# Kernel tuning notes

Hardware: AMD Instinct MI355X
Metric: run time of the kernel (lower is better)

## Reference

```python
import jax, jax.numpy as jnp
import numpy as np

HIDDEN = 1024
NUM_EXPERTS = 64
N_TOKENS = 131072


def setup_inputs() -> dict:
    key = jax.random.key(0)
    k_h, k_w1, k_w2 = jax.random.split(key, 3)
    s1 = 1.0 / np.sqrt(HIDDEN)
    return {
        "h": jax.random.normal(k_h, (N_TOKENS, HIDDEN), dtype=jnp.float32),
        "W1": jax.random.uniform(k_w1, (HIDDEN, HIDDEN), minval=-s1, maxval=s1, dtype=jnp.float32),
        "b1": jnp.zeros((HIDDEN,), jnp.float32),
        "W2": jax.random.uniform(k_w2, (NUM_EXPERTS, HIDDEN), minval=-s1, maxval=s1, dtype=jnp.float32),
        "b2": jnp.zeros((NUM_EXPERTS,), jnp.float32),
        "epoch": 5,
        "top_k": 2,
        "warmup_epochs": 0,
    }


def reference(h, W1, b1, W2, b2, epoch, top_k, warmup_epochs):
    # logits = layer2(tanh(layer1(h)))  -- torch Linear stores weight [out, in]
    logits = jnp.tanh(h @ W1.T + b1) @ W2.T + b2  # [N, E]
    if epoch is None or top_k is None or epoch < warmup_epochs or top_k <= 0:
        return jax.nn.softmax(logits, axis=-1)
    k = min(top_k, NUM_EXPERTS)
    topk_vals, topk_idx = jax.lax.top_k(logits, k)  # [N, k]
    n = logits.shape[0]
    mask = jnp.zeros_like(logits).at[jnp.arange(n)[:, None], topk_idx].set(1.0)
    masked_logits = jnp.where(mask == 0, -jnp.inf, logits)
    return jax.nn.softmax(masked_logits, axis=-1)
```

## Files before the change

### kernel.cpp

```cpp
#include <hip/hip_runtime.h>


constexpr int KT         = 32;
constexpr int A_STRIDE   = 65;
constexpr int W2S_STRIDE = 68;
constexpr int W2S_OFF    = 256 * A_STRIDE;
constexpr int SMEM_FLOATS = W2S_OFF + KT * W2S_STRIDE;

constexpr int WS_B = 0;
constexpr int HS_B = 32768;

constexpr int F32_HS_STRIDE  = 68;
constexpr int F32_WS_STRIDE  = 324;
constexpr int F32_HS_OFF   = 0;
constexpr int F32_WS_OFF   = KT * F32_HS_STRIDE;

typedef __attribute__((ext_vector_type(8))) _Float16 half8;
typedef __attribute__((ext_vector_type(4))) float f32x4;

__device__ __forceinline__ float fast_tanh(float x) {
  float e = __expf(2.0f * x);
  return 1.0f - 2.0f / (e + 1.0f);
}

__device__ __forceinline__ void gload_lds16(const void* g, void* l) {
  __builtin_amdgcn_global_load_lds(
      (const __attribute__((address_space(1))) unsigned int*)g,
      (__attribute__((address_space(3))) unsigned int*)l, 16, 0, 0);
}

__global__ void __launch_bounds__(256)
w1_split(const float* __restrict__ W1, _Float16* __restrict__ ws) {
  const int tid   = blockIdx.x * 256 + threadIdx.x;
  const int col   = tid & 255;
  const int kb    = (tid >> 8) & 3;
  const int chunk = (tid >> 10) & 3;
  const int kt    = tid >> 12;
  const float* src = W1 + (size_t)(chunk * 256 + col) * 1024 + kt * 32 + kb * 8;
  float4 v0 = *(const float4*)src;
  float4 v1 = *(const float4*)(src + 4);
  float vv[8] = {v0.x, v0.y, v0.z, v0.w, v1.x, v1.y, v1.z, v1.w};
  half8 hi, lo;
#pragma unroll
  for (int j = 0; j < 8; ++j) {
    _Float16 a = (_Float16)vv[j];
    hi[j] = a;
    lo[j] = (_Float16)((vv[j] - (float)a) * 2048.0f);
  }
  _Float16* base = ws + (size_t)(kt * 4 + chunk) * 16384;
  *(half8*)(base + kb * 2048 + col * 8)        = hi;
  *(half8*)(base + 8192 + kb * 2048 + col * 8) = lo;
}

__global__ void __launch_bounds__(256, 2)
gating_mfma(const float* __restrict__ h, const _Float16* __restrict__ wsp,
            const float* __restrict__ b1, const float* __restrict__ W2,
            const float* __restrict__ b2, float* __restrict__ out) {
  __shared__ float smem[SMEM_FLOATS];
  char* smb   = (char*)smem;
  float* Al   = smem;
  float* w2s  = smem + W2S_OFF;

  const int t    = threadIdx.x;
  const int lane = t & 63;
  const int wave = t >> 6;
  const int l15  = lane & 15;
  const int l4   = lane >> 4;
  const int tx   = t & 15;
  const int ty   = t >> 4;
  const long rowbase = (long)blockIdx.x * 64;

  float b2v[4];
#pragma unroll
  for (int l = 0; l < 4; ++l) b2v[l] = b2[ty * 4 + l];

  float lacc[4][4];
#pragma unroll
  for (int j = 0; j < 4; ++j)
#pragma unroll
    for (int l = 0; l < 4; ++l) lacc[j][l] = 0.0f;

  for (int chunk = 0; chunk < 4; ++chunk) {
    const int cbase = chunk * 256;

    float b1v[4];
#pragma unroll
    for (int nt = 0; nt < 4; ++nt) b1v[nt] = b1[cbase + wave * 64 + nt * 16 + l15];

    f32x4 acc0[4][4], acc1[4][4];
    {
      f32x4 z = {0.0f, 0.0f, 0.0f, 0.0f};
#pragma unroll
      for (int mt = 0; mt < 4; ++mt)
#pragma unroll
        for (int nt = 0; nt < 4; ++nt) { acc0[mt][nt] = z; acc1[mt][nt] = z; }
    }

    for (int kt = 0; kt < 32; ++kt) {
      __syncthreads();
      {
        const char* srcW = (const char*)(wsp + (size_t)(kt * 4 + chunk) * 16384);
        const int off0 = wave * 8192 + lane * 16;
#pragma unroll
        for (int i = 0; i < 8; ++i) {
          const int off = off0 + i * 1024;
          gload_lds16(srcW + off, smb + WS_B + off);
        }
      }
      {
        const int row = lane;
        const int kb  = wave;
        const float* hp = h + (rowbase + row) * 1024 + kt * 32 + kb * 8;
        float4 v0 = *(const float4*)hp;
        float4 v1 = *(const float4*)(hp + 4);
        float vv[8] = {v0.x, v0.y, v0.z, v0.w, v1.x, v1.y, v1.z, v1.w};
        half8 hi, lo;
#pragma unroll
        for (int j = 0; j < 8; ++j) {
          _Float16 a = (_Float16)vv[j];
          hi[j] = a;
          lo[j] = (_Float16)((vv[j] - (float)a) * 2048.0f);
        }
        *(half8*)(smb + HS_B + kb * 1024 + row * 16)        = hi;
        *(half8*)(smb + HS_B + 4096 + kb * 1024 + row * 16) = lo;
      }
      __syncthreads();

      half8 ah[4], am[4];
#pragma unroll
      for (int mt = 0; mt < 4; ++mt) {
        const int o = HS_B + l4 * 1024 + (mt * 16 + l15) * 16;
        ah[mt] = *(const half8*)(smb + o);
        am[mt] = *(const half8*)(smb + o + 4096);
      }
#pragma unroll
      for (int nt = 0; nt < 4; ++nt) {
        const int o = WS_B + l4 * 4096 + (wave * 64 + nt * 16 + l15) * 16;
        half8 bh = *(const half8*)(smb + o);
        half8 bm = *(const half8*)(smb + o + 16384);
#pragma unroll
        for (int mt = 0; mt < 4; ++mt) {
          acc0[mt][nt] = __builtin_amdgcn_mfma_f32_16x16x32_f16(ah[mt], bh, acc0[mt][nt], 0, 0, 0);
          acc1[mt][nt] = __builtin_amdgcn_mfma_f32_16x16x32_f16(ah[mt], bm, acc1[mt][nt], 0, 0, 0);
          acc1[mt][nt] = __builtin_amdgcn_mfma_f32_16x16x32_f16(am[mt], bh, acc1[mt][nt], 0, 0, 0);
        }
      }
    }

    __syncthreads();
#pragma unroll
    for (int nt = 0; nt < 4; ++nt) {
      const int cloc = wave * 64 + nt * 16 + l15;
#pragma unroll
      for (int mt = 0; mt < 4; ++mt) {
        const int r0 = mt * 16 + l4 * 4;
#pragma unroll
        for (int r = 0; r < 4; ++r) {
          float pre = acc0[mt][nt][r] + acc1[mt][nt][r] * (1.0f / 2048.0f) + b1v[nt];
          Al[cloc * A_STRIDE + r0 + r] = fast_tanh(pre);
        }
      }
    }

    for (int c2 = 0; c2 < 256; c2 += KT) {
      __syncthreads();
      {
        const int e = t >> 2;
        const int cq = (t & 3) * 8;
#pragma unroll
        for (int p = 0; p < 2; ++p) {
          float4 v = *(const float4*)(W2 + (long)e * 1024 + cbase + c2 + cq + p * 4);
          w2s[(cq + p * 4 + 0) * W2S_STRIDE + e] = v.x;
          w2s[(cq + p * 4 + 1) * W2S_STRIDE + e] = v.y;
          w2s[(cq + p * 4 + 2) * W2S_STRIDE + e] = v.z;
          w2s[(cq + p * 4 + 3) * W2S_STRIDE + e] = v.w;
        }
      }
      __syncthreads();
#pragma unroll
      for (int c = 0; c < KT; ++c) {
        const int cloc = c2 + c;
        const float* ap = Al + cloc * A_STRIDE + tx * 4;
        const float a0 = ap[0], a1 = ap[1], a2 = ap[2], a3 = ap[3];
        const float4 wv = *(const float4*)(w2s + c * W2S_STRIDE + ty * 4);
        lacc[0][0] += a0 * wv.x; lacc[0][1] += a0 * wv.y; lacc[0][2] += a0 * wv.z; lacc[0][3] += a0 * wv.w;
        lacc[1][0] += a1 * wv.x; lacc[1][1] += a1 * wv.y; lacc[1][2] += a1 * wv.z; lacc[1][3] += a1 * wv.w;
        lacc[2][0] += a2 * wv.x; lacc[2][1] += a2 * wv.y; lacc[2][2] += a2 * wv.z; lacc[2][3] += a2 * wv.w;
        lacc[3][0] += a3 * wv.x; lacc[3][1] += a3 * wv.y; lacc[3][2] += a3 * wv.z; lacc[3][3] += a3 * wv.w;
      }
    }
  }

  __syncthreads();
#pragma unroll
  for (int j = 0; j < 4; ++j)
#pragma unroll
    for (int l = 0; l < 4; ++l)
      smem[(tx * 4 + j) * 68 + ty * 4 + l] = lacc[j][l] + b2v[l];
  __syncthreads();

  {
    const int row = t >> 2;
    const int sub = t & 3;
    float v1 = -1e30f, v2 = -1e30f;
    int i1 = -1, i2 = -1;
#pragma unroll
    for (int j = 0; j < 16; ++j) {
      const float v = smem[row * 68 + sub * 16 + j];
      const int idx = sub * 16 + j;
      if (v > v1) { v2 = v1; i2 = i1; v1 = v; i1 = idx; }
      else if (v > v2) { v2 = v; i2 = idx; }
    }
#pragma unroll
    for (int off = 1; off <= 2; off <<= 1) {
      const float ov1 = __shfl_xor(v1, off);
      const int   oi1 = __shfl_xor(i1, off);
      const float ov2 = __shfl_xor(v2, off);
      const int   oi2 = __shfl_xor(i2, off);
      if (ov1 > v1) {
        if (v1 > ov2) { v2 = v1; i2 = i1; }
        else          { v2 = ov2; i2 = oi2; }
        v1 = ov1; i1 = oi1;
      } else if (ov1 > v2) {
        v2 = ov1; i2 = oi1;
      }
    }
    const float e2 = __expf(v2 - v1);
    const float inv = 1.0f / (1.0f + e2);
    const float p1 = inv, p2 = e2 * inv;
    float* orow = out + (rowbase + row) * 64 + sub * 16;
#pragma unroll
    for (int q = 0; q < 4; ++q) {
      const int idx0 = sub * 16 + q * 4;
      float4 o;
      o.x = (idx0 + 0 == i1) ? p1 : ((idx0 + 0 == i2) ? p2 : 0.0f);
      o.y = (idx0 + 1 == i1) ? p1 : ((idx0 + 1 == i2) ? p2 : 0.0f);
      o.z = (idx0 + 2 == i1) ? p1 : ((idx0 + 2 == i2) ? p2 : 0.0f);
      o.w = (idx0 + 3 == i1) ? p1 : ((idx0 + 3 == i2) ? p2 : 0.0f);
      *(float4*)(orow + q * 4) = o;
    }
  }
}

__global__ void __launch_bounds__(256, 2)
gating_fused(const float* __restrict__ h, const float* __restrict__ W1,
             const float* __restrict__ b1, const float* __restrict__ W2,
             const float* __restrict__ b2, float* __restrict__ out) {
  __shared__ float smem[SMEM_FLOATS];
  float* hs  = smem + F32_HS_OFF;
  float* ws  = smem + F32_WS_OFF;
  float* Al  = smem;
  float* w2s = smem + W2S_OFF;

  const int t  = threadIdx.x;
  const int tx = t & 15;
  const int ty = t >> 4;
  const long rowbase = (long)blockIdx.x * 64;

  float b2v[4];
#pragma unroll
  for (int l = 0; l < 4; ++l) b2v[l] = b2[ty * 4 + l];

  float lacc[4][4];
#pragma unroll
  for (int j = 0; j < 4; ++j)
#pragma unroll
    for (int l = 0; l < 4; ++l) lacc[j][l] = 0.0f;

  for (int chunk = 0; chunk < 4; ++chunk) {
    const int cbase = chunk * 256;

    float b1v[16];
#pragma unroll
    for (int q = 0; q < 4; ++q) {
      float4 v = *(const float4*)(b1 + cbase + tx * 16 + q * 4);
      b1v[q * 4 + 0] = v.x; b1v[q * 4 + 1] = v.y;
      b1v[q * 4 + 2] = v.z; b1v[q * 4 + 3] = v.w;
    }

    float acc[16][4];
#pragma unroll
    for (int c = 0; c < 16; ++c)
#pragma unroll
      for (int j = 0; j < 4; ++j) acc[c][j] = 0.0f;

    for (int kt = 0; kt < 1024 / KT; ++kt) {
      const int kk = kt * KT;
      __syncthreads();
      {
        const int kq = (t & 7) * 4;
        const int rr = t >> 3;
#pragma unroll
        for (int p = 0; p < 2; ++p) {
          const int r = p * 32 + rr;
          float4 v = *(const float4*)(h + (rowbase + r) * 1024 + kk + kq);
          hs[(kq + 0) * F32_HS_STRIDE + r] = v.x;
          hs[(kq + 1) * F32_HS_STRIDE + r] = v.y;
          hs[(kq + 2) * F32_HS_STRIDE + r] = v.z;
          hs[(kq + 3) * F32_HS_STRIDE + r] = v.w;
        }
#pragma unroll
        for (int p = 0; p < 8; ++p) {
          const int ol = p * 32 + rr;
          float4 v = *(const float4*)(W1 + (long)(cbase + ol) * 1024 + kk + kq);
          float* dst = ws + (ol >> 4) * 20 + (ol & 15);
          dst[(kq + 0) * F32_WS_STRIDE] = v.x;
          dst[(kq + 1) * F32_WS_STRIDE] = v.y;
          dst[(kq + 2) * F32_WS_STRIDE] = v.z;
          dst[(kq + 3) * F32_WS_STRIDE] = v.w;
        }
      }
      __syncthreads();
#pragma unroll
      for (int k = 0; k < KT; ++k) {
        float4 a = *(const float4*)(hs + k * F32_HS_STRIDE + ty * 4);
        const float* wr = ws + k * F32_WS_STRIDE + tx * 20;
        float4 w0 = *(const float4*)(wr + 0);
        float4 w1 = *(const float4*)(wr + 4);
        float4 w2q = *(const float4*)(wr + 8);
        float4 w3 = *(const float4*)(wr + 12);
        float wv[16] = {w0.x, w0.y, w0.z, w0.w, w1.x, w1.y, w1.z, w1.w,
                        w2q.x, w2q.y, w2q.z, w2q.w, w3.x, w3.y, w3.z, w3.w};
#pragma unroll
        for (int c = 0; c < 16; ++c) {
          acc[c][0] += a.x * wv[c];
          acc[c][1] += a.y * wv[c];
          acc[c][2] += a.z * wv[c];
          acc[c][3] += a.w * wv[c];
        }
      }
    }

    __syncthreads();
#pragma unroll
    for (int c = 0; c < 16; ++c) {
      const int cloc = tx * 16 + c;
#pragma unroll
      for (int j = 0; j < 4; ++j)
        Al[cloc * A_STRIDE + ty * 4 + j] = fast_tanh(acc[c][j] + b1v[c]);
    }

    for (int c2 = 0; c2 < 256; c2 += KT) {
      __syncthreads();
      {
        const int e = t >> 2;
        const int cq = (t & 3) * 8;
#pragma unroll
        for (int p = 0; p < 2; ++p) {
          float4 v = *(const float4*)(W2 + (long)e * 1024 + cbase + c2 + cq + p * 4);
          w2s[(cq + p * 4 + 0) * W2S_STRIDE + e] = v.x;
          w2s[(cq + p * 4 + 1) * W2S_STRIDE + e] = v.y;
          w2s[(cq + p * 4 + 2) * W2S_STRIDE + e] = v.z;
          w2s[(cq + p * 4 + 3) * W2S_STRIDE + e] = v.w;
        }
      }
      __syncthreads();
#pragma unroll
      for (int c = 0; c < KT; ++c) {
        const int cloc = c2 + c;
        const float* ap = Al + cloc * A_STRIDE + tx * 4;
        const float a0 = ap[0], a1 = ap[1], a2 = ap[2], a3 = ap[3];
        const float4 wv = *(const float4*)(w2s + c * W2S_STRIDE + ty * 4);
        lacc[0][0] += a0 * wv.x; lacc[0][1] += a0 * wv.y; lacc[0][2] += a0 * wv.z; lacc[0][3] += a0 * wv.w;
        lacc[1][0] += a1 * wv.x; lacc[1][1] += a1 * wv.y; lacc[1][2] += a1 * wv.z; lacc[1][3] += a1 * wv.w;
        lacc[2][0] += a2 * wv.x; lacc[2][1] += a2 * wv.y; lacc[2][2] += a2 * wv.z; lacc[2][3] += a2 * wv.w;
        lacc[3][0] += a3 * wv.x; lacc[3][1] += a3 * wv.y; lacc[3][2] += a3 * wv.z; lacc[3][3] += a3 * wv.w;
      }
    }
  }

  __syncthreads();
#pragma unroll
  for (int j = 0; j < 4; ++j)
#pragma unroll
    for (int l = 0; l < 4; ++l)
      smem[(tx * 4 + j) * 68 + ty * 4 + l] = lacc[j][l] + b2v[l];
  __syncthreads();

  {
    const int row = t >> 2;
    const int sub = t & 3;
    float v1 = -1e30f, v2 = -1e30f;
    int i1 = -1, i2 = -1;
#pragma unroll
    for (int j = 0; j < 16; ++j) {
      const float v = smem[row * 68 + sub * 16 + j];
      const int idx = sub * 16 + j;
      if (v > v1) { v2 = v1; i2 = i1; v1 = v; i1 = idx; }
      else if (v > v2) { v2 = v; i2 = idx; }
    }
#pragma unroll
    for (int off = 1; off <= 2; off <<= 1) {
      const float ov1 = __shfl_xor(v1, off);
      const int   oi1 = __shfl_xor(i1, off);
      const float ov2 = __shfl_xor(v2, off);
      const int   oi2 = __shfl_xor(i2, off);
      if (ov1 > v1) {
        if (v1 > ov2) { v2 = v1; i2 = i1; }
        else          { v2 = ov2; i2 = oi2; }
        v1 = ov1; i1 = oi1;
      } else if (ov1 > v2) {
        v2 = ov1; i2 = oi1;
      }
    }
    const float e2 = __expf(v2 - v1);
    const float inv = 1.0f / (1.0f + e2);
    const float p1 = inv, p2 = e2 * inv;
    float* orow = out + (rowbase + row) * 64 + sub * 16;
#pragma unroll
    for (int q = 0; q < 4; ++q) {
      const int idx0 = sub * 16 + q * 4;
      float4 o;
      o.x = (idx0 + 0 == i1) ? p1 : ((idx0 + 0 == i2) ? p2 : 0.0f);
      o.y = (idx0 + 1 == i1) ? p1 : ((idx0 + 1 == i2) ? p2 : 0.0f);
      o.z = (idx0 + 2 == i1) ? p1 : ((idx0 + 2 == i2) ? p2 : 0.0f);
      o.w = (idx0 + 3 == i1) ? p1 : ((idx0 + 3 == i2) ? p2 : 0.0f);
      *(float4*)(orow + q * 4) = o;
    }
  }
}

extern "C" void kernel_launch(void* const* d_in, const int* in_sizes, int n_in,
                              void* d_out, int out_size, void* d_ws, size_t ws_size,
                              hipStream_t stream) {
  const float* h  = (const float*)d_in[0];
  const float* W1 = (const float*)d_in[1];
  const float* b1 = (const float*)d_in[2];
  const float* W2 = (const float*)d_in[3];
  const float* b2 = (const float*)d_in[4];
  float* out = (float*)d_out;
  if (d_ws && ws_size >= (size_t)4 * 1024 * 1024) {
    _Float16* wsp = (_Float16*)d_ws;
    w1_split<<<dim3(512), dim3(256), 0, stream>>>(W1, wsp);
    gating_mfma<<<dim3(131072 / 64), dim3(256), 0, stream>>>(h, wsp, b1, W2, b2, out);
  } else {
    gating_fused<<<dim3(131072 / 64), dim3(256), 0, stream>>>(h, W1, b1, W2, b2, out);
  }
}
```

Baseline: 1.761 ms.

## Use 128-row blocks of 8 waves with double-buffered W1 staging

The MFMA gating kernel now processes 128 tokens per block with 512 threads arranged as a 2x4 wave grid. Each W1 hi/lo tile is shared by twice as many rows. The W1 tile is double-buffered in LDS so the next tile's async load overlaps the current MFMAs, leaving one barrier per k-step. h fragments are loaded straight into registers and split into fp16 hi/lo there, which drops the LDS round trip for activations. The costs are higher register pressure from the prefetched h values and a larger LDS footprint (about 142 KB) that may cap blocks per CU.

```diff
diff --git a/kernel.cpp b/kernel.cpp
--- a/kernel.cpp
+++ b/kernel.cpp
@@ -2,17 +2,16 @@
 
 
 constexpr int KT         = 32;
+constexpr int AS2        = 131;
+constexpr int W2S_STRIDE = 68;
+constexpr int W2S_OFF2   = 256 * AS2;
+constexpr int SMEM2_FLOATS = W2S_OFF2 + KT * W2S_STRIDE;
+
 constexpr int A_STRIDE   = 65;
-constexpr int W2S_STRIDE = 68;
-constexpr int W2S_OFF    = 256 * A_STRIDE;
-constexpr int SMEM_FLOATS = W2S_OFF + KT * W2S_STRIDE;
-
-constexpr int WS_B = 0;
-constexpr int HS_B = 32768;
-
+constexpr int F32_W2S_OFF = 256 * A_STRIDE;
+constexpr int F32_SMEM   = F32_W2S_OFF + KT * W2S_STRIDE;
 constexpr int F32_HS_STRIDE  = 68;
 constexpr int F32_WS_STRIDE  = 324;
-constexpr int F32_HS_OFF   = 0;
 constexpr int F32_WS_OFF   = KT * F32_HS_STRIDE;
 
 typedef __attribute__((ext_vector_type(8))) _Float16 half8;
@@ -27,6 +26,16 @@
   __builtin_amdgcn_global_load_lds(
       (const __attribute__((address_space(1))) unsigned int*)g,
       (__attribute__((address_space(3))) unsigned int*)l, 16, 0, 0);
+}
+
+__device__ __forceinline__ void split8(const float4 a, const float4 b, half8& hi, half8& lo) {
+  float v[8] = {a.x, a.y, a.z, a.w, b.x, b.y, b.z, b.w};
+#pragma unroll
+  for (int i = 0; i < 8; ++i) {
+    _Float16 x = (_Float16)v[i];
+    hi[i] = x;
+    lo[i] = (_Float16)((v[i] - (float)x) * 2048.0f);
+  }
 }
 
 __global__ void __launch_bounds__(256)
@@ -52,27 +61,37 @@
   *(half8*)(base + 8192 + kb * 2048 + col * 8) = lo;
 }
 
-__global__ void __launch_bounds__(256, 2)
-gating_mfma(const float* __restrict__ h, const _Float16* __restrict__ wsp,
-            const float* __restrict__ b1, const float* __restrict__ W2,
-            const float* __restrict__ b2, float* __restrict__ out) {
-  __shared__ float smem[SMEM_FLOATS];
+__global__ void __launch_bounds__(512, 2)
+gating_mfma2(const float* __restrict__ h, const _Float16* __restrict__ wsp,
+             const float* __restrict__ b1, const float* __restrict__ W2,
+             const float* __restrict__ b2, float* __restrict__ out) {
+  __shared__ float smem[SMEM2_FLOATS];
   char* smb   = (char*)smem;
   float* Al   = smem;
-  float* w2s  = smem + W2S_OFF;
+  float* w2s  = smem + W2S_OFF2;
 
   const int t    = threadIdx.x;
   const int lane = t & 63;
   const int wave = t >> 6;
+  const int wm   = wave >> 2;
+  const int wn   = wave & 3;
   const int l15  = lane & 15;
   const int l4   = lane >> 4;
-  const int tx   = t & 15;
-  const int ty   = t >> 4;
-  const long rowbase = (long)blockIdx.x * 64;
+  const long rowbase = (long)blockIdx.x * 128;
+
+  const float* hp[4];
+#pragma unroll
+  for (int mt = 0; mt < 4; ++mt)
+    hp[mt] = h + (rowbase + wm * 64 + mt * 16 + l15) * 1024 + l4 * 8;
+
+  const int g   = t >> 8;
+  const int u   = t & 255;
+  const int tx  = u & 15;
+  const int ty2 = u >> 4;
 
   float b2v[4];
 #pragma unroll
-  for (int l = 0; l < 4; ++l) b2v[l] = b2[ty * 4 + l];
+  for (int l = 0; l < 4; ++l) b2v[l] = b2[ty2 * 4 + l];
 
   float lacc[4][4];
 #pragma unroll
@@ -85,7 +104,7 @@
 
     float b1v[4];
 #pragma unroll
-    for (int nt = 0; nt < 4; ++nt) b1v[nt] = b1[cbase + wave * 64 + nt * 16 + l15];
+    for (int nt = 0; nt < 4; ++nt) b1v[nt] = b1[cbase + wn * 64 + nt * 16 + l15];
 
     f32x4 acc0[4][4], acc1[4][4];
     {
@@ -96,48 +115,39 @@
         for (int nt = 0; nt < 4; ++nt) { acc0[mt][nt] = z; acc1[mt][nt] = z; }
     }
 
+    auto stage = [&](int kt, int buf) {
+      const char* srcW = (const char*)wsp + (((size_t)kt * 4 + chunk) << 15);
+      char* dst = smb + buf * 32768;
+      const int o0 = t * 16;
+#pragma unroll
+      for (int i = 0; i < 4; ++i)
+        gload_lds16(srcW + o0 + i * 8192, dst + o0 + i * 8192);
+    };
+
+    __syncthreads();
+    stage(0, 0);
+    __syncthreads();
+
     for (int kt = 0; kt < 32; ++kt) {
-      __syncthreads();
-      {
-        const char* srcW = (const char*)(wsp + (size_t)(kt * 4 + chunk) * 16384);
-        const int off0 = wave * 8192 + lane * 16;
-#pragma unroll
-        for (int i = 0; i < 8; ++i) {
-          const int off = off0 + i * 1024;
-          gload_lds16(srcW + off, smb + WS_B + off);
-        }
-      }
-      {
-        const int row = lane;
-        const int kb  = wave;
-        const float* hp = h + (rowbase + row) * 1024 + kt * 32 + kb * 8;
-        float4 v0 = *(const float4*)hp;
-        float4 v1 = *(const float4*)(hp + 4);
-        float vv[8] = {v0.x, v0.y, v0.z, v0.w, v1.x, v1.y, v1.z, v1.w};
-        half8 hi, lo;
-#pragma unroll
-        for (int j = 0; j < 8; ++j) {
-          _Float16 a = (_Float16)vv[j];
-          hi[j] = a;
-          lo[j] = (_Float16)((vv[j] - (float)a) * 2048.0f);
-        }
-        *(half8*)(smb + HS_B + kb * 1024 + row * 16)        = hi;
-        *(half8*)(smb + HS_B + 4096 + kb * 1024 + row * 16) = lo;
-      }
-      __syncthreads();
+      float4 hr0[4], hr1[4];
+#pragma unroll
+      for (int mt = 0; mt < 4; ++mt) {
+        const float* p = hp[mt] + kt * 32;
+        hr0[mt] = *(const float4*)p;
+        hr1[mt] = *(const float4*)(p + 4);
+      }
+      if (kt < 31) stage(kt + 1, (kt + 1) & 1);
 
       half8 ah[4], am[4];
 #pragma unroll
-      for (int mt = 0; mt < 4; ++mt) {
-        const int o = HS_B + l4 * 1024 + (mt * 16 + l15) * 16;
-        ah[mt] = *(const half8*)(smb + o);
-        am[mt] = *(const half8*)(smb + o + 4096);
-      }
+      for (int mt = 0; mt < 4; ++mt) split8(hr0[mt], hr1[mt], ah[mt], am[mt]);
+
+      const char* bufp = smb + (kt & 1) * 32768 + l4 * 4096;
 #pragma unroll
       for (int nt = 0; nt < 4; ++nt) {
-        const int o = WS_B + l4 * 4096 + (wave * 64 + nt * 16 + l15) * 16;
-        half8 bh = *(const half8*)(smb + o);
-        half8 bm = *(const half8*)(smb + o + 16384);
+        const char* bp = bufp + (wn * 64 + nt * 16 + l15) * 16;
+        half8 bh = *(const half8*)bp;
+        half8 bm = *(const half8*)(bp + 16384);
 #pragma unroll
         for (int mt = 0; mt < 4; ++mt) {
           acc0[mt][nt] = __builtin_amdgcn_mfma_f32_16x16x32_f16(ah[mt], bh, acc0[mt][nt], 0, 0, 0);
@@ -145,19 +155,19 @@
           acc1[mt][nt] = __builtin_amdgcn_mfma_f32_16x16x32_f16(am[mt], bh, acc1[mt][nt], 0, 0, 0);
         }
       }
-    }
-
-    __syncthreads();
+      __syncthreads();
+    }
+
 #pragma unroll
     for (int nt = 0; nt < 4; ++nt) {
-      const int cloc = wave * 64 + nt * 16 + l15;
+      const int cloc = wn * 64 + nt * 16 + l15;
 #pragma unroll
       for (int mt = 0; mt < 4; ++mt) {
-        const int r0 = mt * 16 + l4 * 4;
+        const int r0 = wm * 64 + mt * 16 + l4 * 4;
 #pragma unroll
         for (int r = 0; r < 4; ++r) {
           float pre = acc0[mt][nt][r] + acc1[mt][nt][r] * (1.0f / 2048.0f) + b1v[nt];
-          Al[cloc * A_STRIDE + r0 + r] = fast_tanh(pre);
+          Al[cloc * AS2 + r0 + r] = fast_tanh(pre);
         }
       }
     }
@@ -165,24 +175,21 @@
     for (int c2 = 0; c2 < 256; c2 += KT) {
       __syncthreads();
       {
-        const int e = t >> 2;
-        const int cq = (t & 3) * 8;
-#pragma unroll
-        for (int p = 0; p < 2; ++p) {
-          float4 v = *(const float4*)(W2 + (long)e * 1024 + cbase + c2 + cq + p * 4);
-          w2s[(cq + p * 4 + 0) * W2S_STRIDE + e] = v.x;
-          w2s[(cq + p * 4 + 1) * W2S_STRIDE + e] = v.y;
-          w2s[(cq + p * 4 + 2) * W2S_STRIDE + e] = v.z;
-          w2s[(cq + p * 4 + 3) * W2S_STRIDE + e] = v.w;
-        }
+        const int e  = t >> 3;
+        const int cq = (t & 7) * 4;
+        float4 v = *(const float4*)(W2 + (long)e * 1024 + cbase + c2 + cq);
+        w2s[(cq + 0) * W2S_STRIDE + e] = v.x;
+        w2s[(cq + 1) * W2S_STRIDE + e] = v.y;
+        w2s[(cq + 2) * W2S_STRIDE + e] = v.z;
+        w2s[(cq + 3) * W2S_STRIDE + e] = v.w;
       }
       __syncthreads();
 #pragma unroll
       for (int c = 0; c < KT; ++c) {
         const int cloc = c2 + c;
-        const float* ap = Al + cloc * A_STRIDE + tx * 4;
+        const float* ap = Al + cloc * AS2 + g * 64 + tx * 4;
         const float a0 = ap[0], a1 = ap[1], a2 = ap[2], a3 = ap[3];
-        const float4 wv = *(const float4*)(w2s + c * W2S_STRIDE + ty * 4);
+        const float4 wv = *(const float4*)(w2s + c * W2S_STRIDE + ty2 * 4);
         lacc[0][0] += a0 * wv.x; lacc[0][1] += a0 * wv.y; lacc[0][2] += a0 * wv.z; lacc[0][3] += a0 * wv.w;
         lacc[1][0] += a1 * wv.x; lacc[1][1] += a1 * wv.y; lacc[1][2] += a1 * wv.z; lacc[1][3] += a1 * wv.w;
         lacc[2][0] += a2 * wv.x; lacc[2][1] += a2 * wv.y; lacc[2][2] += a2 * wv.z; lacc[2][3] += a2 * wv.w;
@@ -196,12 +203,12 @@
   for (int j = 0; j < 4; ++j)
 #pragma unroll
     for (int l = 0; l < 4; ++l)
-      smem[(tx * 4 + j) * 68 + ty * 4 + l] = lacc[j][l] + b2v[l];
+      smem[(g * 64 + tx * 4 + j) * 68 + ty2 * 4 + l] = lacc[j][l] + b2v[l];
   __syncthreads();
 
   {
-    const int row = t >> 2;
-    const int sub = t & 3;
+    const int row = g * 64 + (u >> 2);
+    const int sub = u & 3;
     float v1 = -1e30f, v2 = -1e30f;
     int i1 = -1, i2 = -1;
 #pragma unroll
@@ -246,11 +253,11 @@
 gating_fused(const float* __restrict__ h, const float* __restrict__ W1,
              const float* __restrict__ b1, const float* __restrict__ W2,
              const float* __restrict__ b2, float* __restrict__ out) {
-  __shared__ float smem[SMEM_FLOATS];
-  float* hs  = smem + F32_HS_OFF;
+  __shared__ float smem[F32_SMEM];
+  float* hs  = smem;
   float* ws  = smem + F32_WS_OFF;
   float* Al  = smem;
-  float* w2s = smem + W2S_OFF;
+  float* w2s = smem + F32_W2S_OFF;
 
   const int t  = threadIdx.x;
   const int tx = t & 15;
@@ -432,7 +439,7 @@
   if (d_ws && ws_size >= (size_t)4 * 1024 * 1024) {
     _Float16* wsp = (_Float16*)d_ws;
     w1_split<<<dim3(512), dim3(256), 0, stream>>>(W1, wsp);
-    gating_mfma<<<dim3(131072 / 64), dim3(256), 0, stream>>>(h, wsp, b1, W2, b2, out);
+    gating_mfma2<<<dim3(131072 / 128), dim3(512), 0, stream>>>(h, wsp, b1, W2, b2, out);
   } else {
     gating_fused<<<dim3(131072 / 64), dim3(256), 0, stream>>>(h, W1, b1, W2, b2, out);
   }
```

Result: slower. 2.544 ms (+44.5%).
